# Kernel optimization log

Measured on AMD Instinct MI355X. Metric: run time of the kernel, lower is better.

The kernel has to match this reference:

```python
import jax, jax.numpy as jnp
import numpy as np

N = 50000      # nodes
E = 400000     # edges (before self-loops)
F_IN = 256     # input_dim
HID = 64       # hidden_dim (per-head)
H = 4          # heads
OUT = 16       # output_dim
NEG_SLOPE = 0.2


def _gat_layer(x, W, a_src, a_dst, b, src, dst):
    # x: [N, Fin], W: [Fin, H*HID], a_src/a_dst: [H, HID], b: [H*HID]
    n = x.shape[0]
    h = (x @ W).reshape(n, H, HID)                        # [N,H,D]
    es = jnp.einsum('nhd,hd->nh', h, a_src)               # [N,H]
    ed = jnp.einsum('nhd,hd->nh', h, a_dst)               # [N,H]
    e = jax.nn.leaky_relu(es[src] + ed[dst], NEG_SLOPE)   # [E,H]
    m = jax.ops.segment_max(e, dst, num_segments=n)       # [N,H] segment softmax (stable)
    m = jnp.where(jnp.isfinite(m), m, 0.0)
    p = jnp.exp(e - m[dst])
    s = jax.ops.segment_sum(p, dst, num_segments=n)
    alpha = p / (s[dst] + 1e-16)                          # [E,H]
    out = jax.ops.segment_sum(h[src] * alpha[:, :, None], dst, num_segments=n)  # [N,H,D]
    return out.reshape(n, H * HID) + b


def setup_inputs() -> dict:
    key = jax.random.key(0)
    ks = jax.random.split(key, 24)
    lin = lambda k, i, o: (jax.random.normal(k, (i, o), jnp.float32) / np.sqrt(i)).astype(jnp.float32)
    att = lambda k: (jax.random.normal(k, (H, HID), jnp.float32) * 0.1).astype(jnp.float32)
    FH = H * HID  # 256
    inp = {
        'x': jax.random.normal(ks[0], (N, F_IN), jnp.float32),
        'edge_index': jax.random.randint(ks[1], (2, E), 0, N, dtype=jnp.int64),
        'W1': lin(ks[2], F_IN, FH), 'a1_src': att(ks[3]), 'a1_dst': att(ks[4]), 'b1': jnp.zeros((FH,), jnp.float32),
        'W2': lin(ks[5], FH, FH),   'a2_src': att(ks[6]), 'a2_dst': att(ks[7]), 'b2': jnp.zeros((FH,), jnp.float32),
        'W3': lin(ks[8], FH, FH),   'a3_src': att(ks[9]), 'a3_dst': att(ks[10]), 'b3': jnp.zeros((FH,), jnp.float32),
        'pW1': lin(ks[11], FH, HID), 'pb1': jnp.zeros((HID,), jnp.float32),
        'pW2': lin(ks[12], HID, HID), 'pb2': jnp.zeros((HID,), jnp.float32),
        'cW1': lin(ks[13], FH, HID), 'cb1': jnp.zeros((HID,), jnp.float32),
        'cW2': lin(ks[14], HID, OUT), 'cb2': jnp.zeros((OUT,), jnp.float32),
    }
    return inp


def reference(x, edge_index, W1, a1_src, a1_dst, b1, W2, a2_src, a2_dst, b2,
              W3, a3_src, a3_dst, b3, pW1, pb1, pW2, pb2, cW1, cb1, cW2, cb2):
    n = x.shape[0]
    loop = jnp.arange(n, dtype=edge_index.dtype)          # PyG GATConv adds self-loops
    src = jnp.concatenate([edge_index[0], loop])
    dst = jnp.concatenate([edge_index[1], loop])
    h = jax.nn.elu(_gat_layer(x, W1, a1_src, a1_dst, b1, src, dst))
    h = jax.nn.elu(_gat_layer(h, W2, a2_src, a2_dst, b2, src, dst))
    h = _gat_layer(h, W3, a3_src, a3_dst, b3, src, dst)   # [N, 256]
    logits = jax.nn.relu(h @ cW1 + cb1) @ cW2 + cb2       # classifier (dropout inactive, eval)
    proj = jax.nn.relu(h @ pW1 + pb1) @ pW2 + pb2         # projection head
    return jax.nn.log_softmax(logits, axis=1), proj
```

## Files before the change

### kernel.cpp

```cpp
#include <hip/hip_runtime.h>
#include <hip/hip_bf16.h>

#define NN 50000
#define EE 400000
#define TE (EE + NN)
#define SCAN_B ((NN + 255) / 256)
#define CONV_B (NN * 256 / 4 / 256)
#define PREP_B ((PO_TOTAL + 255) / 256)
#define GEMM_BX ((NN + 127) / 128)
#define SCAT_X  880
#define DSTRIDE 64

typedef float f4 __attribute__((ext_vector_type(4)));
typedef __bf16 b8 __attribute__((ext_vector_type(8)));
typedef unsigned short us8 __attribute__((ext_vector_type(8)));

__device__ __forceinline__ float b2f(unsigned short u) {
    union { unsigned int i; float f; } c; c.i = ((unsigned int)u) << 16; return c.f;
}
__device__ __forceinline__ unsigned short f2b(float x) {
    union { unsigned int i; float f; } c; c.f = x;
    unsigned int i = c.i;
    return (unsigned short)((i + 0x7FFFu + ((i >> 16) & 1u)) >> 16);
}
__device__ __forceinline__ int clampi(int v, int lo, int hi) {
    return v < lo ? lo : (v > hi ? hi : v);
}
__device__ __forceinline__ int uclamp(int v) {
    unsigned u = (unsigned)v;
    return (int)(u < (unsigned)(NN - 1) ? u : (unsigned)(NN - 1));
}

#define PO_WT    0
#define PO_ATT   196608
#define PO_BT    198912
#define PO_BIAS  231680
#define PO_PW2   231808
#define PO_PB2   235904
#define PO_CW2   235968
#define PO_CB2   236992
#define PO_BT2   237008
#define PO_BIAS2 253392
#define PO_TOTAL 253520

__device__ __forceinline__ int detect_xbf(const unsigned int* xw, int tid, int* sm) {
    if (tid < 64) {
        int cnt = 0;
#pragma unroll
        for (int k = 0; k < 4; k++) {
            int i = tid + k * 64;
            unsigned short lo = (unsigned short)(xw[i] & 0xFFFFu);
            int e = (lo >> 7) & 0xFF;
            if (e >= 120 && e <= 132) cnt++;
        }
#pragma unroll
        for (int off = 1; off < 64; off <<= 1) cnt += __shfl_xor(cnt, off, 64);
        if (tid == 0) *sm = (cnt >= 128) ? 1 : 0;
    }
    __syncthreads();
    return *sm;
}
__device__ __forceinline__ int detect_e64(const int* ei, int tid, int* sm) {
    if (tid < 64) {
        int bad = (tid < 16 && ei[2 * tid + 1] != 0) ? 1 : 0;
        unsigned long long anybad = __ballot(bad != 0);
        if (tid == 0) *sm = (anybad == 0ULL) ? 1 : 0;
    }
    __syncthreads();
    return *sm;
}

__device__ __forceinline__ float ldf(const void* p, int i, int bf) {
    return bf ? b2f(((const unsigned short*)p)[i]) : ((const float*)p)[i];
}

__global__ __launch_bounds__(256) void convx_prep_kernel(
    const void* __restrict__ xsrc, unsigned short* __restrict__ dst,
    int* __restrict__ cursor,
    const void* W1, const void* W2, const void* W3,
    const void* as1, const void* ad1, const void* b1,
    const void* as2, const void* ad2, const void* b2,
    const void* as3, const void* ad3, const void* b3,
    const void* pW1, const void* pb1, const void* pW2, const void* pb2,
    const void* cW1, const void* cb1, const void* cW2, const void* cb2,
    unsigned short* __restrict__ P) {
    __shared__ int sm;
    int tid = threadIdx.x;
    int bf = detect_xbf((const unsigned int*)xsrc, tid, &sm);
    int b = blockIdx.x;
    if (b < CONV_B) {
        int i = b * 256 + tid;
        if (b < SCAN_B && i < NN) cursor[i] = 0;
        if (i >= NN * 256 / 4) return;
        if (bf) {
            ((ushort4*)dst)[i] = ((const ushort4*)xsrc)[i];
        } else {
            float4 v = ((const float4*)xsrc)[i];
            ushort4 o; o.x = f2b(v.x); o.y = f2b(v.y); o.z = f2b(v.z); o.w = f2b(v.w);
            ((ushort4*)dst)[i] = o;
        }
        return;
    }
    int idx = (b - CONV_B) * 256 + tid;
    if (idx >= PO_TOTAL) return;
    float v;
    if (idx < PO_ATT) {
        int l = idx / 65536, r = idx % 65536;
        int n = r >> 8, k = r & 255;
        const void* W = (l == 0) ? W1 : (l == 1) ? W2 : W3;
        v = ldf(W, k * 256 + n, bf);
    } else if (idx < PO_BT) {
        int r = idx - PO_ATT;
        int l = r / 768, w = r % 768, which = w >> 8, j = w & 255;
        const void* s;
        if (which == 0) s = (l == 0) ? as1 : (l == 1) ? as2 : as3;
        else if (which == 1) s = (l == 0) ? ad1 : (l == 1) ? ad2 : ad3;
        else s = (l == 0) ? b1 : (l == 1) ? b2 : b3;
        v = ldf(s, j, bf);
    } else if (idx < PO_BIAS) {
        int r3 = idx - PO_BT;
        int r = r3 >> 8, k = r3 & 255;
        v = (r < 64) ? ldf(cW1, k * 64 + r, bf) : ldf(pW1, k * 64 + (r - 64), bf);
    } else if (idx < PO_PW2) {
        int r = idx - PO_BIAS;
        v = (r < 64) ? ldf(cb1, r, bf) : ldf(pb1, r - 64, bf);
    } else if (idx < PO_PB2) {
        v = ldf(pW2, idx - PO_PW2, bf);
    } else if (idx < PO_CW2) {
        v = ldf(pb2, idx - PO_PB2, bf);
    } else if (idx < PO_CB2) {
        v = ldf(cW2, idx - PO_CW2, bf);
    } else if (idx < PO_BT2) {
        v = ldf(cb2, idx - PO_CB2, bf);
    } else if (idx < PO_BIAS2) {
        int r2 = idx - PO_BT2;
        int r = r2 >> 7, k = r2 & 127;
        if (r < 16) v = (k < 64) ? ldf(cW2, k * 16 + r, bf) : 0.f;
        else if (r < 80) v = (k >= 64) ? ldf(pW2, (k - 64) * 64 + (r - 16), bf) : 0.f;
        else v = 0.f;
    } else {
        int r = idx - PO_BIAS2;
        v = (r < 16) ? ldf(cb2, r, bf) : (r < 80 ? ldf(pb2, r - 16, bf) : 0.f);
    }
    P[idx] = f2b(v);
}

__device__ __forceinline__ void edge_decode(const int* __restrict__ ei, int mode64, int e,
                                            int& src, int& dst) {
    if (e < EE) {
        if (mode64) { src = ei[2 * e]; dst = ei[2 * EE + 2 * e]; }
        else        { src = ei[e];     dst = ei[EE + e]; }
        src = clampi(src, 0, NN - 1);
        dst = clampi(dst, 0, NN - 1);
    } else {
        src = dst = e - EE;
    }
}

__device__ __forceinline__ void async_ld16(const unsigned short* g, unsigned short* l) {
    __builtin_amdgcn_global_load_lds(
        (const __attribute__((address_space(1))) unsigned int*)g,
        (__attribute__((address_space(3))) unsigned int*)l, 16, 0, 0);
}

__global__ __launch_bounds__(256) void gemm_bt_kernel(
    const unsigned short* __restrict__ A, const unsigned short* __restrict__ Bt,
    unsigned short* __restrict__ C, int M,
    const unsigned short* __restrict__ asrc, const unsigned short* __restrict__ adst,
    float* __restrict__ es, float* __restrict__ ed,
    const int* __restrict__ ei, int* __restrict__ cursor, int* __restrict__ srcs, int scat) {
    const int K = 256, Nc = 256;
    __shared__ unsigned short smem[16384];
    unsigned short* As0 = smem;
    unsigned short* Bs0 = smem + 8192;
    int tid = threadIdx.x;
    if (scat && blockIdx.x >= GEMM_BX) {
        __shared__ int sm;
        int mode64 = detect_e64(ei, tid, &sm);
        int c = (blockIdx.x - GEMM_BX) + SCAT_X * blockIdx.y;
        int e = c * 256 + tid;
        if (e >= TE) return;
        int src, dst;
        edge_decode(ei, mode64, e, src, dst);
        int pos = atomicAdd(&cursor[dst], 1);
        if (pos > DSTRIDE - 1) pos = DSTRIDE - 1;
        srcs[dst * DSTRIDE + pos] = src;
        return;
    }
    int lane = tid & 63;
    int wave = tid >> 6;
    int wr = wave >> 1, wc = wave & 1;
    int m0 = blockIdx.x * 128;
    int n0 = blockIdx.y * 128;
    f4 acc[4][4];
#pragma unroll
    for (int i = 0; i < 4; i++)
#pragma unroll
        for (int j = 0; j < 4; j++) acc[i][j] = (f4){0.f, 0.f, 0.f, 0.f};

    int rin = lane >> 2;
    int qsl = lane & 3;
    int qg  = qsl ^ ((rin >> 1) & 3);
    int rsel = lane & 15;
    int q16 = lane >> 4;
    int slotq = q16 ^ ((rsel >> 1) & 3);

    auto stage = [&](int b, int kt) {
#pragma unroll
        for (int t = 0; t < 4; t++) {
            int seg = wave * 4 + t;
            if (seg < 8) {
                int gm = m0 + seg * 16 + rin;
                if (gm > M - 1) gm = M - 1;
                async_ld16(A + (size_t)gm * K + kt + qg * 8, &As0[b * 4096 + seg * 512]);
            } else {
                int gn = n0 + (seg - 8) * 16 + rin;
                async_ld16(Bt + (size_t)gn * K + kt + qg * 8, &Bs0[b * 4096 + (seg - 8) * 512]);
            }
        }
    };

    const int nk = K >> 5;
    stage(0, 0);
    __syncthreads();
    for (int s = 0; s < nk; s++) {
        int cur = s & 1;
        if (s + 1 < nk) stage(cur ^ 1, (s + 1) << 5);
        b8 af[4], bfv[4];
#pragma unroll
        for (int i = 0; i < 4; i++) {
            af[i]  = *(const b8*)(&As0[cur * 4096 + (wr * 64 + i * 16 + rsel) * 32 + slotq * 8]);
            bfv[i] = *(const b8*)(&Bs0[cur * 4096 + (wc * 64 + i * 16 + rsel) * 32 + slotq * 8]);
        }
#pragma unroll
        for (int i = 0; i < 4; i++)
#pragma unroll
            for (int j = 0; j < 4; j++)
                acc[i][j] = __builtin_amdgcn_mfma_f32_16x16x32_bf16(af[i], bfv[j], acc[i][j], 0, 0, 0);
        __syncthreads();
    }
    int cl = lane & 15, rq = lane >> 4;
    {
        int head = blockIdx.y * 2 + wc;
        float asv[4], adv[4];
#pragma unroll
        for (int j = 0; j < 4; j++) {
            asv[j] = b2f(asrc[head * 64 + j * 16 + cl]);
            adv[j] = b2f(adst[head * 64 + j * 16 + cl]);
        }
#pragma unroll
        for (int i = 0; i < 4; i++) {
            float pes[4], ped[4];
#pragma unroll
            for (int r = 0; r < 4; r++) {
                float se = 0.f, de = 0.f;
#pragma unroll
                for (int j = 0; j < 4; j++) {
                    se += acc[i][j][r] * asv[j];
                    de += acc[i][j][r] * adv[j];
                }
                pes[r] = se; ped[r] = de;
            }
#pragma unroll
            for (int off = 1; off < 16; off <<= 1) {
#pragma unroll
                for (int r = 0; r < 4; r++) {
                    pes[r] += __shfl_xor(pes[r], off, 64);
                    ped[r] += __shfl_xor(ped[r], off, 64);
                }
            }
            if (cl == 0) {
#pragma unroll
                for (int r = 0; r < 4; r++) {
                    int row = m0 + wr * 64 + i * 16 + rq * 4 + r;
                    if (row < M) {
                        es[(size_t)row * 4 + head] = pes[r];
                        ed[(size_t)row * 4 + head] = ped[r];
                    }
                }
            }
        }
    }
    unsigned short* Cs = smem;
#pragma unroll
    for (int j = 0; j < 4; j++) {
        int col = wc * 64 + j * 16 + cl;
        int chunk = col >> 3, cw = col & 7;
#pragma unroll
        for (int i = 0; i < 4; i++) {
#pragma unroll
            for (int r = 0; r < 4; r++) {
                int row = wr * 64 + i * 16 + rq * 4 + r;
                Cs[row * 128 + ((chunk ^ (row & 15)) << 3) + cw] = f2b(acc[i][j][r]);
            }
        }
    }
    __syncthreads();
#pragma unroll
    for (int it = 0; it < 8; it++) {
        int row = it * 16 + (tid >> 4);
        int chunk = tid & 15;
        int gr = m0 + row;
        if (gr < M) {
            us8 v = *(const us8*)(&Cs[row * 128 + ((chunk ^ (row & 15)) << 3)]);
            *(us8*)(&C[(size_t)gr * Nc + n0 + chunk * 8]) = v;
        }
    }
}

__global__ __launch_bounds__(256) void gemm_final_kernel(
    const unsigned short* __restrict__ A, const unsigned short* __restrict__ Bt1,
    const unsigned short* __restrict__ bias1, const unsigned short* __restrict__ B2g,
    const unsigned short* __restrict__ bias2,
    float* __restrict__ flog, float* __restrict__ fproj, int M) {
    const int K = 256;
    __shared__ unsigned short smem[32768];
    unsigned short* As0 = smem;
    unsigned short* Bs0 = smem + 8192;
    unsigned short* T   = smem;
    unsigned short* B2s = smem + 16384;
    int tid = threadIdx.x;
    int lane = tid & 63;
    int wave = tid >> 6;
    int wr = wave >> 1, wc = wave & 1;
    int m0 = blockIdx.x * 128;
    f4 acc[4][4];
#pragma unroll
    for (int i = 0; i < 4; i++)
#pragma unroll
        for (int j = 0; j < 4; j++) acc[i][j] = (f4){0.f, 0.f, 0.f, 0.f};

    int rin = lane >> 2;
    int qsl = lane & 3;
    int qg  = qsl ^ ((rin >> 1) & 3);
    int rsel = lane & 15;
    int q16 = lane >> 4;
    int slotq = q16 ^ ((rsel >> 1) & 3);

#pragma unroll
    for (int t = 0; t < 8; t++) {
        int row = t * 16 + wave * 4 + (lane >> 4);
        int chunk = lane & 15;
        async_ld16(B2g + row * 128 + ((chunk ^ (row & 15)) << 3),
                   B2s + (t * 16 + wave * 4) * 128);
    }

    auto stage = [&](int b, int kt) {
#pragma unroll
        for (int t = 0; t < 4; t++) {
            int seg = wave * 4 + t;
            if (seg < 8) {
                int gm = m0 + seg * 16 + rin;
                if (gm < M)
                    async_ld16(A + (size_t)gm * K + kt + qg * 8, &As0[b * 4096 + seg * 512]);
            } else {
                int r = (seg - 8) * 16 + rin;
                async_ld16(Bt1 + (size_t)r * K + kt + qg * 8, &Bs0[b * 4096 + (seg - 8) * 512]);
            }
        }
    };

    stage(0, 0);
    __syncthreads();
    for (int s = 0; s < 8; s++) {
        int cur = s & 1;
        if (s + 1 < 8) stage(cur ^ 1, (s + 1) << 5);
        b8 af[4], bfv[4];
#pragma unroll
        for (int i = 0; i < 4; i++) {
            af[i]  = *(const b8*)(&As0[cur * 4096 + (wr * 64 + i * 16 + rsel) * 32 + slotq * 8]);
            bfv[i] = *(const b8*)(&Bs0[cur * 4096 + (wc * 64 + i * 16 + rsel) * 32 + slotq * 8]);
        }
#pragma unroll
        for (int i = 0; i < 4; i++)
#pragma unroll
            for (int j = 0; j < 4; j++)
                acc[i][j] = __builtin_amdgcn_mfma_f32_16x16x32_bf16(af[i], bfv[j], acc[i][j], 0, 0, 0);
        __syncthreads();
    }

    int cl = lane & 15, rq = lane >> 4;
#pragma unroll
    for (int j = 0; j < 4; j++) {
        int col = wc * 64 + j * 16 + cl;
        float bv = b2f(bias1[col]);
        int chunk = col >> 3, cr = col & 7;
#pragma unroll
        for (int i = 0; i < 4; i++) {
#pragma unroll
            for (int r = 0; r < 4; r++) {
                int row = wr * 64 + i * 16 + rq * 4 + r;
                float v = fmaxf(acc[i][j][r] + bv, 0.0f);
                T[row * 128 + ((chunk ^ (row & 15)) << 3) + cr] = f2b(v);
            }
        }
    }
    __syncthreads();

    f4 acc2[4][4];
#pragma unroll
    for (int i = 0; i < 4; i++)
#pragma unroll
        for (int j = 0; j < 4; j++) acc2[i][j] = (f4){0.f, 0.f, 0.f, 0.f};
#pragma unroll
    for (int s2 = 0; s2 < 4; s2++) {
        int kc = s2 * 4 + q16;
        b8 af2[4], bf2[4];
#pragma unroll
        for (int i = 0; i < 4; i++) {
            int row = wr * 64 + i * 16 + rsel;
            af2[i] = *(const b8*)(&T[row * 128 + ((kc ^ (row & 15)) << 3)]);
        }
#pragma unroll
        for (int j = 0; j < 4; j++) {
            int col = wc * 64 + j * 16 + rsel;
            bf2[j] = *(const b8*)(&B2s[col * 128 + ((kc ^ (col & 15)) << 3)]);
        }
#pragma unroll
        for (int i = 0; i < 4; i++)
#pragma unroll
            for (int j = 0; j < 4; j++)
                acc2[i][j] = __builtin_amdgcn_mfma_f32_16x16x32_bf16(af2[i], bf2[j], acc2[i][j], 0, 0, 0);
    }

#pragma unroll
    for (int i = 0; i < 4; i++) {
#pragma unroll
        for (int r = 0; r < 4; r++) {
            int row = m0 + wr * 64 + i * 16 + rq * 4 + r;
            if (row >= M) continue;
            if (wc == 0) {
                float lv = acc2[i][0][r] + b2f(bias2[cl]);
                float mx = lv;
#pragma unroll
                for (int off = 1; off < 16; off <<= 1) mx = fmaxf(mx, __shfl_xor(mx, off, 64));
                float se = __expf(lv - mx);
#pragma unroll
                for (int off = 1; off < 16; off <<= 1) se += __shfl_xor(se, off, 64);
                flog[(size_t)row * 16 + cl] = lv - mx - __logf(se);
#pragma unroll
                for (int j = 1; j < 4; j++) {
                    float pv = acc2[i][j][r] + b2f(bias2[j * 16 + cl]);
                    fproj[(size_t)row * 64 + j * 16 + cl - 16] = pv;
                }
            } else {
                float pv = acc2[i][0][r] + b2f(bias2[64 + cl]);
                fproj[(size_t)row * 64 + 48 + cl] = pv;
            }
        }
    }
}

__global__ __launch_bounds__(256) void aggr_kernel(
    const unsigned short* __restrict__ H, const float* __restrict__ es,
    const float* __restrict__ ed,
    const int* __restrict__ cursor, const int* __restrict__ srcs,
    const unsigned short* __restrict__ bias, unsigned short* __restrict__ out, int N, int elu) {
    int gw = (blockIdx.x * 256 + threadIdx.x) >> 6;
    int lane = threadIdx.x & 63;
    if (gw >= N) return;
    int half = lane >> 5;
    int lh = lane & 31;
    int ch = lh << 3;
    int head = lh >> 3;
    int j0 = gw * DSTRIDE;
    int d = cursor[gw];
    d = d < DSTRIDE ? d : DSTRIDE;
    int j1 = j0 + d;
    float edh = ed[gw * 4 + head];
    float a0 = 0.f, a1 = 0.f, a2 = 0.f, a3 = 0.f;
    float a4 = 0.f, a5 = 0.f, a6 = 0.f, a7 = 0.f;
    float sw = 0.f;
    int nfull8 = d & ~7;
    for (int t = 0; t < nfull8; t += 8) {
        int base = j0 + t + half * 4;
        int s0 = uclamp(srcs[base]), s1 = uclamp(srcs[base + 1]);
        int s2 = uclamp(srcs[base + 2]), s3 = uclamp(srcs[base + 3]);
        float e0 = es[s0 * 4 + head], e1 = es[s1 * 4 + head];
        float e2 = es[s2 * 4 + head], e3 = es[s3 * 4 + head];
        us8 h0 = *(const us8*)(H + (size_t)s0 * 256 + ch);
        us8 h1 = *(const us8*)(H + (size_t)s1 * 256 + ch);
        us8 h2 = *(const us8*)(H + (size_t)s2 * 256 + ch);
        us8 h3 = *(const us8*)(H + (size_t)s3 * 256 + ch);
        float v0 = e0 + edh; v0 = v0 > 0.f ? v0 : 0.2f * v0;
        float v1 = e1 + edh; v1 = v1 > 0.f ? v1 : 0.2f * v1;
        float v2 = e2 + edh; v2 = v2 > 0.f ? v2 : 0.2f * v2;
        float v3 = e3 + edh; v3 = v3 > 0.f ? v3 : 0.2f * v3;
        float w0 = __expf(v0), w1 = __expf(v1), w2 = __expf(v2), w3 = __expf(v3);
        sw += (w0 + w1) + (w2 + w3);
        a0 += w0 * b2f(h0[0]) + w1 * b2f(h1[0]) + w2 * b2f(h2[0]) + w3 * b2f(h3[0]);
        a1 += w0 * b2f(h0[1]) + w1 * b2f(h1[1]) + w2 * b2f(h2[1]) + w3 * b2f(h3[1]);
        a2 += w0 * b2f(h0[2]) + w1 * b2f(h1[2]) + w2 * b2f(h2[2]) + w3 * b2f(h3[2]);
        a3 += w0 * b2f(h0[3]) + w1 * b2f(h1[3]) + w2 * b2f(h2[3]) + w3 * b2f(h3[3]);
        a4 += w0 * b2f(h0[4]) + w1 * b2f(h1[4]) + w2 * b2f(h2[4]) + w3 * b2f(h3[4]);
        a5 += w0 * b2f(h0[5]) + w1 * b2f(h1[5]) + w2 * b2f(h2[5]) + w3 * b2f(h3[5]);
        a6 += w0 * b2f(h0[6]) + w1 * b2f(h1[6]) + w2 * b2f(h2[6]) + w3 * b2f(h3[6]);
        a7 += w0 * b2f(h0[7]) + w1 * b2f(h1[7]) + w2 * b2f(h2[7]) + w3 * b2f(h3[7]);
    }
    int jt = j0 + nfull8;
    if (j1 - jt >= 4) {
        int base = jt + half * 2;
        int s0 = uclamp(srcs[base]), s1 = uclamp(srcs[base + 1]);
        float e0 = es[s0 * 4 + head], e1 = es[s1 * 4 + head];
        us8 h0 = *(const us8*)(H + (size_t)s0 * 256 + ch);
        us8 h1 = *(const us8*)(H + (size_t)s1 * 256 + ch);
        float v0 = e0 + edh; v0 = v0 > 0.f ? v0 : 0.2f * v0;
        float v1 = e1 + edh; v1 = v1 > 0.f ? v1 : 0.2f * v1;
        float w0 = __expf(v0), w1 = __expf(v1);
        sw += w0 + w1;
        a0 += w0 * b2f(h0[0]) + w1 * b2f(h1[0]);
        a1 += w0 * b2f(h0[1]) + w1 * b2f(h1[1]);
        a2 += w0 * b2f(h0[2]) + w1 * b2f(h1[2]);
        a3 += w0 * b2f(h0[3]) + w1 * b2f(h1[3]);
        a4 += w0 * b2f(h0[4]) + w1 * b2f(h1[4]);
        a5 += w0 * b2f(h0[5]) + w1 * b2f(h1[5]);
        a6 += w0 * b2f(h0[6]) + w1 * b2f(h1[6]);
        a7 += w0 * b2f(h0[7]) + w1 * b2f(h1[7]);
        jt += 4;
    }
    for (int j = jt + half; j < j1; j += 2) {
        int sA = uclamp(srcs[j]);
        float eA = es[sA * 4 + head];
        us8 hA = *(const us8*)(H + (size_t)sA * 256 + ch);
        float vA = eA + edh; vA = vA > 0.f ? vA : 0.2f * vA;
        float wA = __expf(vA);
        sw += wA;
        a0 += wA * b2f(hA[0]); a1 += wA * b2f(hA[1]);
        a2 += wA * b2f(hA[2]); a3 += wA * b2f(hA[3]);
        a4 += wA * b2f(hA[4]); a5 += wA * b2f(hA[5]);
        a6 += wA * b2f(hA[6]); a7 += wA * b2f(hA[7]);
    }
    sw += __shfl_xor(sw, 32, 64);
    a0 += __shfl_xor(a0, 32, 64); a1 += __shfl_xor(a1, 32, 64);
    a2 += __shfl_xor(a2, 32, 64); a3 += __shfl_xor(a3, 32, 64);
    a4 += __shfl_xor(a4, 32, 64); a5 += __shfl_xor(a5, 32, 64);
    a6 += __shfl_xor(a6, 32, 64); a7 += __shfl_xor(a7, 32, 64);
    if (half == 0) {
        float rs = 1.f / (sw + 1e-16f);
        us8 bv = *(const us8*)(bias + ch);
        float r0 = a0 * rs + b2f(bv[0]), r1 = a1 * rs + b2f(bv[1]);
        float r2 = a2 * rs + b2f(bv[2]), r3 = a3 * rs + b2f(bv[3]);
        float r4 = a4 * rs + b2f(bv[4]), r5 = a5 * rs + b2f(bv[5]);
        float r6 = a6 * rs + b2f(bv[6]), r7 = a7 * rs + b2f(bv[7]);
        if (elu) {
            r0 = r0 > 0.f ? r0 : __expf(r0) - 1.f;
            r1 = r1 > 0.f ? r1 : __expf(r1) - 1.f;
            r2 = r2 > 0.f ? r2 : __expf(r2) - 1.f;
            r3 = r3 > 0.f ? r3 : __expf(r3) - 1.f;
            r4 = r4 > 0.f ? r4 : __expf(r4) - 1.f;
            r5 = r5 > 0.f ? r5 : __expf(r5) - 1.f;
            r6 = r6 > 0.f ? r6 : __expf(r6) - 1.f;
            r7 = r7 > 0.f ? r7 : __expf(r7) - 1.f;
        }
        us8 o;
        o[0] = f2b(r0); o[1] = f2b(r1); o[2] = f2b(r2); o[3] = f2b(r3);
        o[4] = f2b(r4); o[5] = f2b(r5); o[6] = f2b(r6); o[7] = f2b(r7);
        *(us8*)(out + (size_t)gw * 256 + ch) = o;
    }
}

extern "C" void kernel_launch(void* const* d_in, const int* in_sizes, int n_in,
                              void* d_out, int out_size, void* d_ws, size_t ws_size,
                              hipStream_t stream) {
    (void)in_sizes; (void)n_in; (void)out_size; (void)ws_size;
    const int* ei = (const int*)d_in[1];

    char* p = (char*)d_ws;
    auto take = [&](size_t bytes) -> void* {
        void* r = (void*)p;
        p += (bytes + 255) & ~(size_t)255;
        return r;
    };
    int* cursor = (int*)take((size_t)NN * 4);
    int* srcs   = (int*)take((size_t)NN * DSTRIDE * 4);
    float* es   = (float*)take((size_t)NN * 16);
    float* ed   = (float*)take((size_t)NN * 16);
    unsigned short* bufH = (unsigned short*)take((size_t)NN * 256 * 2);
    unsigned short* buf1 = (unsigned short*)take((size_t)NN * 256 * 2);
    unsigned short* buf2 = (unsigned short*)take((size_t)NN * 256 * 2);
    unsigned short* P    = (unsigned short*)take((size_t)PO_TOTAL * 2);
    unsigned short* xb = buf2;

    convx_prep_kernel<<<CONV_B + PREP_B, 256, 0, stream>>>(
        d_in[0], xb, cursor,
        d_in[2], d_in[6], d_in[10],
        d_in[3], d_in[4], d_in[5],
        d_in[7], d_in[8], d_in[9],
        d_in[11], d_in[12], d_in[13],
        d_in[14], d_in[15], d_in[16], d_in[17],
        d_in[18], d_in[19], d_in[20], d_in[21],
        P);

    const unsigned short* X = xb;
    unsigned short* outbuf[3] = {buf1, buf2, buf1};
    for (int l = 0; l < 3; l++) {
        const unsigned short* Wt  = P + PO_WT + l * 65536;
        const unsigned short* asr = P + PO_ATT + l * 768;
        const unsigned short* adr = P + PO_ATT + l * 768 + 256;
        const unsigned short* bcb = P + PO_ATT + l * 768 + 512;
        dim3 g = (l == 0) ? dim3(GEMM_BX + SCAT_X, 2) : dim3(GEMM_BX, 2);
        gemm_bt_kernel<<<g, 256, 0, stream>>>(
            X, Wt, bufH, NN, asr, adr, es, ed,
            ei, cursor, srcs, (l == 0) ? 1 : 0);
        aggr_kernel<<<12500, 256, 0, stream>>>(bufH, es, ed, cursor, srcs, bcb, outbuf[l], NN, (l < 2) ? 1 : 0);
        X = outbuf[l];
    }
    float* out0 = (float*)d_out;
    float* out1 = out0 + (size_t)NN * 16;
    gemm_final_kernel<<<(NN + 127) / 128, 256, 0, stream>>>(
        X, P + PO_BT, P + PO_BIAS, P + PO_BT2, P + PO_BIAS2, out0, out1, NN);
}
```

Before: 355.7 us.

## Retile GEMM to 64x256 blocks covering all heads, stage es/ed in LDS

The layer GEMM moves from 128x128 tiles on a 2-wide column grid to 64-row tiles spanning all 256 output columns, so each wave owns one attention head and A is read once per row block. The es/ed attention logits are collected in shared memory and written as one float4 per row instead of scattered scalar stores. The scatter blocks become a 1D grid. In exchange the block count rises, B tile traffic per block doubles, and LDS use per block grows.

```diff
diff --git a/kernel.cpp b/kernel.cpp
--- a/kernel.cpp
+++ b/kernel.cpp
@@ -7,8 +7,8 @@
 #define SCAN_B ((NN + 255) / 256)
 #define CONV_B (NN * 256 / 4 / 256)
 #define PREP_B ((PO_TOTAL + 255) / 256)
-#define GEMM_BX ((NN + 127) / 128)
-#define SCAT_X  880
+#define GEMM_BX ((NN + 63) / 64)
+#define SCAT_TOT ((TE + 255) / 256)
 #define DSTRIDE 64
 
 typedef float f4 __attribute__((ext_vector_type(4)));
@@ -170,14 +170,14 @@
     float* __restrict__ es, float* __restrict__ ed,
     const int* __restrict__ ei, int* __restrict__ cursor, int* __restrict__ srcs, int scat) {
     const int K = 256, Nc = 256;
-    __shared__ unsigned short smem[16384];
+    __shared__ unsigned short smem[20480];
     unsigned short* As0 = smem;
-    unsigned short* Bs0 = smem + 8192;
+    unsigned short* Bs0 = smem + 4096;
     int tid = threadIdx.x;
     if (scat && blockIdx.x >= GEMM_BX) {
         __shared__ int sm;
         int mode64 = detect_e64(ei, tid, &sm);
-        int c = (blockIdx.x - GEMM_BX) + SCAT_X * blockIdx.y;
+        int c = blockIdx.x - GEMM_BX;
         int e = c * 256 + tid;
         if (e >= TE) return;
         int src, dst;
@@ -189,9 +189,7 @@
     }
     int lane = tid & 63;
     int wave = tid >> 6;
-    int wr = wave >> 1, wc = wave & 1;
-    int m0 = blockIdx.x * 128;
-    int n0 = blockIdx.y * 128;
+    int m0 = blockIdx.x * 64;
     f4 acc[4][4];
 #pragma unroll
     for (int i = 0; i < 4; i++)
@@ -206,17 +204,16 @@
     int slotq = q16 ^ ((rsel >> 1) & 3);
 
     auto stage = [&](int b, int kt) {
+        {
+            int gm = m0 + wave * 16 + rin;
+            if (gm > M - 1) gm = M - 1;
+            async_ld16(A + (size_t)gm * K + kt + qg * 8, &As0[b * 2048 + wave * 512]);
+        }
 #pragma unroll
         for (int t = 0; t < 4; t++) {
             int seg = wave * 4 + t;
-            if (seg < 8) {
-                int gm = m0 + seg * 16 + rin;
-                if (gm > M - 1) gm = M - 1;
-                async_ld16(A + (size_t)gm * K + kt + qg * 8, &As0[b * 4096 + seg * 512]);
-            } else {
-                int gn = n0 + (seg - 8) * 16 + rin;
-                async_ld16(Bt + (size_t)gn * K + kt + qg * 8, &Bs0[b * 4096 + (seg - 8) * 512]);
-            }
+            int gn = seg * 16 + rin;
+            async_ld16(Bt + (size_t)gn * K + kt + qg * 8, &Bs0[b * 8192 + seg * 512]);
         }
     };
 
@@ -229,8 +226,8 @@
         b8 af[4], bfv[4];
 #pragma unroll
         for (int i = 0; i < 4; i++) {
-            af[i]  = *(const b8*)(&As0[cur * 4096 + (wr * 64 + i * 16 + rsel) * 32 + slotq * 8]);
-            bfv[i] = *(const b8*)(&Bs0[cur * 4096 + (wc * 64 + i * 16 + rsel) * 32 + slotq * 8]);
+            af[i]  = *(const b8*)(&As0[cur * 2048 + (i * 16 + rsel) * 32 + slotq * 8]);
+            bfv[i] = *(const b8*)(&Bs0[cur * 8192 + (wave * 64 + i * 16 + rsel) * 32 + slotq * 8]);
         }
 #pragma unroll
         for (int i = 0; i < 4; i++)
@@ -240,8 +237,10 @@
         __syncthreads();
     }
     int cl = lane & 15, rq = lane >> 4;
+    float* es_s = (float*)smem;
+    float* ed_s = (float*)smem + 256;
     {
-        int head = blockIdx.y * 2 + wc;
+        int head = wave;
         float asv[4], adv[4];
 #pragma unroll
         for (int j = 0; j < 4; j++) {
@@ -272,38 +271,45 @@
             if (cl == 0) {
 #pragma unroll
                 for (int r = 0; r < 4; r++) {
-                    int row = m0 + wr * 64 + i * 16 + rq * 4 + r;
-                    if (row < M) {
-                        es[(size_t)row * 4 + head] = pes[r];
-                        ed[(size_t)row * 4 + head] = ped[r];
-                    }
+                    int row = i * 16 + rq * 4 + r;
+                    es_s[row * 4 + head] = pes[r];
+                    ed_s[row * 4 + head] = ped[r];
                 }
             }
         }
     }
-    unsigned short* Cs = smem;
+    unsigned short* Cs = Bs0;
 #pragma unroll
     for (int j = 0; j < 4; j++) {
-        int col = wc * 64 + j * 16 + cl;
+        int col = wave * 64 + j * 16 + cl;
         int chunk = col >> 3, cw = col & 7;
 #pragma unroll
         for (int i = 0; i < 4; i++) {
 #pragma unroll
             for (int r = 0; r < 4; r++) {
-                int row = wr * 64 + i * 16 + rq * 4 + r;
-                Cs[row * 128 + ((chunk ^ (row & 15)) << 3) + cw] = f2b(acc[i][j][r]);
+                int row = i * 16 + rq * 4 + r;
+                Cs[row * 256 + ((chunk ^ (row & 31)) << 3) + cw] = f2b(acc[i][j][r]);
             }
         }
     }
     __syncthreads();
+    if (tid < 64) {
+        int row = tid;
+        if (m0 + row < M)
+            ((float4*)es)[m0 + row] = *(const float4*)(&es_s[row * 4]);
+    } else if (tid < 128) {
+        int row = tid - 64;
+        if (m0 + row < M)
+            ((float4*)ed)[m0 + row] = *(const float4*)(&ed_s[row * 4]);
+    }
 #pragma unroll
     for (int it = 0; it < 8; it++) {
-        int row = it * 16 + (tid >> 4);
-        int chunk = tid & 15;
+        int row = it * 8 + (tid >> 5);
+        int chunk = tid & 31;
         int gr = m0 + row;
         if (gr < M) {
-            us8 v = *(const us8*)(&Cs[row * 128 + ((chunk ^ (row & 15)) << 3)]);
-            *(us8*)(&C[(size_t)gr * Nc + n0 + chunk * 8]) = v;
+            us8 v = *(const us8*)(&Cs[row * 256 + ((chunk ^ (row & 31)) << 3)]);
+            *(us8*)(&C[(size_t)gr * Nc + chunk * 8]) = v;
         }
     }
 }
@@ -598,8 +604,8 @@
         const unsigned short* asr = P + PO_ATT + l * 768;
         const unsigned short* adr = P + PO_ATT + l * 768 + 256;
         const unsigned short* bcb = P + PO_ATT + l * 768 + 512;
-        dim3 g = (l == 0) ? dim3(GEMM_BX + SCAT_X, 2) : dim3(GEMM_BX, 2);
-        gemm_bt_kernel<<<g, 256, 0, stream>>>(
+        int gx = (l == 0) ? (GEMM_BX + SCAT_TOT) : GEMM_BX;
+        gemm_bt_kernel<<<gx, 256, 0, stream>>>(
             X, Wt, bufH, NN, asr, adr, es, ed,
             ei, cursor, srcs, (l == 0) ? 1 : 0);
         aggr_kernel<<<12500, 256, 0, stream>>>(bufH, es, ed, cursor, srcs, bcb, outbuf[l], NN, (l < 2) ? 1 : 0);
```

Measured after the change: 374.7 us. 1.05x slower.

## Fuse fp32-to-bf16 input conversion into the first-layer GEMM A-tile loads

Applied to the files above, without the earlier changes.

Drops the separate pass that converts x to bf16 and writes it to a workspace buffer. The layer-1 GEMM now loads raw x into registers in two of its four waves, converts each fp32 element to bf16, and writes the result into the LDS A tile after the MFMA step. The other two waves keep loading B asynchronously. This removes the write and re-read of a bf16 copy of x. In exchange the GEMM reads fp32 twice across its two column blocks, and the A loads are synchronous register loads instead of async global-to-LDS copies.

```diff
diff --git a/kernel.cpp b/kernel.cpp
--- a/kernel.cpp
+++ b/kernel.cpp
@@ -5,7 +5,6 @@
 #define EE 400000
 #define TE (EE + NN)
 #define SCAN_B ((NN + 255) / 256)
-#define CONV_B (NN * 256 / 4 / 256)
 #define PREP_B ((PO_TOTAL + 255) / 256)
 #define GEMM_BX ((NN + 127) / 128)
 #define SCAT_X  880
@@ -74,9 +73,8 @@
     return bf ? b2f(((const unsigned short*)p)[i]) : ((const float*)p)[i];
 }
 
-__global__ __launch_bounds__(256) void convx_prep_kernel(
-    const void* __restrict__ xsrc, unsigned short* __restrict__ dst,
-    int* __restrict__ cursor,
+__global__ __launch_bounds__(256) void prep_kernel(
+    const void* __restrict__ xsrc, int* __restrict__ cursor,
     const void* W1, const void* W2, const void* W3,
     const void* as1, const void* ad1, const void* b1,
     const void* as2, const void* ad2, const void* b2,
@@ -87,21 +85,8 @@
     __shared__ int sm;
     int tid = threadIdx.x;
     int bf = detect_xbf((const unsigned int*)xsrc, tid, &sm);
-    int b = blockIdx.x;
-    if (b < CONV_B) {
-        int i = b * 256 + tid;
-        if (b < SCAN_B && i < NN) cursor[i] = 0;
-        if (i >= NN * 256 / 4) return;
-        if (bf) {
-            ((ushort4*)dst)[i] = ((const ushort4*)xsrc)[i];
-        } else {
-            float4 v = ((const float4*)xsrc)[i];
-            ushort4 o; o.x = f2b(v.x); o.y = f2b(v.y); o.z = f2b(v.z); o.w = f2b(v.w);
-            ((ushort4*)dst)[i] = o;
-        }
-        return;
-    }
-    int idx = (b - CONV_B) * 256 + tid;
+    int idx = blockIdx.x * 256 + tid;
+    if (idx < NN) cursor[idx] = 0;
     if (idx >= PO_TOTAL) return;
     float v;
     if (idx < PO_ATT) {
@@ -164,7 +149,8 @@
 }
 
 __global__ __launch_bounds__(256) void gemm_bt_kernel(
-    const unsigned short* __restrict__ A, const unsigned short* __restrict__ Bt,
+    const unsigned short* __restrict__ A, const void* __restrict__ Xraw, int amode,
+    const unsigned short* __restrict__ Bt,
     unsigned short* __restrict__ C, int M,
     const unsigned short* __restrict__ asrc, const unsigned short* __restrict__ adst,
     float* __restrict__ es, float* __restrict__ ed,
@@ -187,6 +173,9 @@
         srcs[dst * DSTRIDE + pos] = src;
         return;
     }
+    __shared__ int smf;
+    int bfx = 1;
+    if (amode) bfx = detect_xbf((const unsigned int*)Xraw, tid, &smf);
     int lane = tid & 63;
     int wave = tid >> 6;
     int wr = wave >> 1, wc = wave & 1;
@@ -205,27 +194,74 @@
     int q16 = lane >> 4;
     int slotq = q16 ^ ((rsel >> 1) & 3);
 
-    auto stage = [&](int b, int kt) {
-#pragma unroll
-        for (int t = 0; t < 4; t++) {
-            int seg = wave * 4 + t;
-            if (seg < 8) {
-                int gm = m0 + seg * 16 + rin;
-                if (gm > M - 1) gm = M - 1;
-                async_ld16(A + (size_t)gm * K + kt + qg * 8, &As0[b * 4096 + seg * 512]);
+    f4 raf[4][2];
+    us8 rab[4];
+
+    auto stageL = [&](int b, int kt) {
+        if (amode) {
+            if (wave < 2) {
+#pragma unroll
+                for (int t = 0; t < 4; t++) {
+                    int seg = wave * 4 + t;
+                    int gm = m0 + seg * 16 + rin;
+                    if (gm > M - 1) gm = M - 1;
+                    if (bfx) {
+                        rab[t] = *(const us8*)((const unsigned short*)Xraw + (size_t)gm * K + kt + qg * 8);
+                    } else {
+                        const float* xf = (const float*)Xraw + (size_t)gm * K + kt + qg * 8;
+                        raf[t][0] = *(const f4*)xf;
+                        raf[t][1] = *(const f4*)(xf + 4);
+                    }
+                }
             } else {
-                int gn = n0 + (seg - 8) * 16 + rin;
-                async_ld16(Bt + (size_t)gn * K + kt + qg * 8, &Bs0[b * 4096 + (seg - 8) * 512]);
+#pragma unroll
+                for (int t = 0; t < 4; t++) {
+                    int seg = wave * 4 + t;
+                    int gn = n0 + (seg - 8) * 16 + rin;
+                    async_ld16(Bt + (size_t)gn * K + kt + qg * 8, &Bs0[b * 4096 + (seg - 8) * 512]);
+                }
+            }
+        } else {
+#pragma unroll
+            for (int t = 0; t < 4; t++) {
+                int seg = wave * 4 + t;
+                if (seg < 8) {
+                    int gm = m0 + seg * 16 + rin;
+                    if (gm > M - 1) gm = M - 1;
+                    async_ld16(A + (size_t)gm * K + kt + qg * 8, &As0[b * 4096 + seg * 512]);
+                } else {
+                    int gn = n0 + (seg - 8) * 16 + rin;
+                    async_ld16(Bt + (size_t)gn * K + kt + qg * 8, &Bs0[b * 4096 + (seg - 8) * 512]);
+                }
             }
         }
     };
+    auto stageW = [&](int b) {
+        if (amode && wave < 2) {
+#pragma unroll
+            for (int t = 0; t < 4; t++) {
+                int seg = wave * 4 + t;
+                us8 v;
+                if (bfx) {
+                    v = rab[t];
+                } else {
+                    v[0] = f2b(raf[t][0][0]); v[1] = f2b(raf[t][0][1]);
+                    v[2] = f2b(raf[t][0][2]); v[3] = f2b(raf[t][0][3]);
+                    v[4] = f2b(raf[t][1][0]); v[5] = f2b(raf[t][1][1]);
+                    v[6] = f2b(raf[t][1][2]); v[7] = f2b(raf[t][1][3]);
+                }
+                *(us8*)(&As0[b * 4096 + seg * 512 + lane * 8]) = v;
+            }
+        }
+    };
 
     const int nk = K >> 5;
-    stage(0, 0);
+    stageL(0, 0);
+    stageW(0);
     __syncthreads();
     for (int s = 0; s < nk; s++) {
         int cur = s & 1;
-        if (s + 1 < nk) stage(cur ^ 1, (s + 1) << 5);
+        if (s + 1 < nk) stageL(cur ^ 1, (s + 1) << 5);
         b8 af[4], bfv[4];
 #pragma unroll
         for (int i = 0; i < 4; i++) {
@@ -237,6 +273,7 @@
 #pragma unroll
             for (int j = 0; j < 4; j++)
                 acc[i][j] = __builtin_amdgcn_mfma_f32_16x16x32_bf16(af[i], bfv[j], acc[i][j], 0, 0, 0);
+        if (s + 1 < nk) stageW(cur ^ 1);
         __syncthreads();
     }
     int cl = lane & 15, rq = lane >> 4;
@@ -579,10 +616,9 @@
     unsigned short* buf1 = (unsigned short*)take((size_t)NN * 256 * 2);
     unsigned short* buf2 = (unsigned short*)take((size_t)NN * 256 * 2);
     unsigned short* P    = (unsigned short*)take((size_t)PO_TOTAL * 2);
-    unsigned short* xb = buf2;
-
-    convx_prep_kernel<<<CONV_B + PREP_B, 256, 0, stream>>>(
-        d_in[0], xb, cursor,
+
+    prep_kernel<<<PREP_B, 256, 0, stream>>>(
+        d_in[0], cursor,
         d_in[2], d_in[6], d_in[10],
         d_in[3], d_in[4], d_in[5],
         d_in[7], d_in[8], d_in[9],
@@ -591,7 +627,7 @@
         d_in[18], d_in[19], d_in[20], d_in[21],
         P);
 
-    const unsigned short* X = xb;
+    const unsigned short* X = nullptr;
     unsigned short* outbuf[3] = {buf1, buf2, buf1};
     for (int l = 0; l < 3; l++) {
         const unsigned short* Wt  = P + PO_WT + l * 65536;
@@ -600,7 +636,8 @@
         const unsigned short* bcb = P + PO_ATT + l * 768 + 512;
         dim3 g = (l == 0) ? dim3(GEMM_BX + SCAT_X, 2) : dim3(GEMM_BX, 2);
         gemm_bt_kernel<<<g, 256, 0, stream>>>(
-            X, Wt, bufH, NN, asr, adr, es, ed,
+            X, (l == 0) ? d_in[0] : nullptr, (l == 0) ? 1 : 0,
+            Wt, bufH, NN, asr, adr, es, ed,
             ei, cursor, srcs, (l == 0) ? 1 : 0);
         aggr_kernel<<<12500, 256, 0, stream>>>(bufH, es, ed, cursor, srcs, bcb, outbuf[l], NN, (l < 2) ? 1 : 0);
         X = outbuf[l];
```

Result: slower. 369.7 us (+3.9%).
